# Kernel tuning notes

Hardware: AMD Instinct MI355X
Metric: run time of the kernel (lower is better)

Reference implementation:

```python
import jax, jax.numpy as jnp
import numpy as np

B = 8; NPC = 12500; N = B * NPC
L = 10.0; RES = 0.7; K = 16
IN_CH = 64; H1 = 68; H2 = 128; RNN = 128; ATTN = 32; E4 = 4 * RNN
EPS = 1e-5


def _knn_np(refs, queries, k):
    out = np.empty((queries.shape[0], k), dtype=np.int64)
    r2 = (refs * refs).sum(1)
    for s in range(0, queries.shape[0], 2048):
        q = queries[s:s + 2048]
        d2 = (q * q).sum(1)[:, None] - 2.0 * q @ refs.T + r2[None, :]
        out[s:s + q.shape[0]] = np.argpartition(d2, k, axis=1)[:, :k]
    return out


def setup_inputs():
    rng = np.random.default_rng(0)
    pos = rng.uniform(0.0, L, (N, 3)).astype(np.float32)
    batch = np.repeat(np.arange(B), NPC).astype(np.int32)
    x = (0.5 * rng.standard_normal((N, IN_CH))).astype(np.float32)
    refl = rng.uniform(0.0, 1.0, N).astype(np.float32)
    # voxel-grid sampling: one representative point per occupied voxel per cloud
    G = int(np.ceil(L / RES)) + 1
    v = np.floor(pos / RES).astype(np.int64)
    vkey = ((batch.astype(np.int64) * G + v[:, 0]) * G + v[:, 1]) * G + v[:, 2]
    _, first = np.unique(vkey, return_index=True)
    idx = np.sort(first)
    M = idx.shape[0]
    # per-cloud brute-force KNN (k neighbors in full set for every sampled point)
    src_list = []
    for b in range(B):
        qi = idx[(idx >= b * NPC) & (idx < (b + 1) * NPC)]
        src_list.append(_knn_np(pos[b * NPC:(b + 1) * NPC], pos[qi], K) + b * NPC)
    src = np.concatenate(src_list, 0).reshape(-1)
    tgt = np.repeat(np.arange(M), K)
    edge_index = np.stack([src, tgt]).astype(np.int32)

    def W(*s):
        return jnp.asarray((0.05 * rng.standard_normal(s)).astype(np.float32))

    def zeros(c):
        return jnp.zeros((c,), jnp.float32)

    def bnp(c):  # packed inference-mode BN params: [gamma, beta, mean, var]
        return jnp.asarray(np.stack([1.0 + 0.1 * rng.standard_normal(c), 0.1 * rng.standard_normal(c), 0.1 * rng.standard_normal(c), 1.0 + 0.1 * rng.uniform(0.0, 1.0, c)]).astype(np.float32))

    def dwp(c):  # depthwise k=1 conv = per-channel [weight, bias]
        return jnp.asarray(np.stack([1.0 + 0.1 * rng.standard_normal(c), 0.1 * rng.standard_normal(c)]).astype(np.float32))

    gum = -np.log(-np.log(rng.uniform(1e-6, 1.0 - 1e-6, (B, 2))))
    return dict(
        x=jnp.asarray(x), pos=jnp.asarray(pos), reflectance=jnp.asarray(refl),
        gumbel=jnp.asarray(gum.astype(np.float32)),
        gate_w1=W(4, H1), gate_b1=zeros(H1), gate_w2=W(H1, H1), gate_b2=zeros(H1),
        gate_wg=W(H1, 2), gate_bg=jnp.asarray(np.array([0.0, 2.0], np.float32)),
        loc_w1=W(H1, H2), loc_b1=zeros(H2), loc_w2=W(H2, H2), loc_b2=zeros(H2),
        attn_w1=W(H2, ATTN), attn_b1=zeros(ATTN), attn_w2=W(ATTN),
        exp_w=W(RNN, E4), exp_b=zeros(E4), exp_bn=bnp(E4),
        ds1_dw=dwp(E4), ds1_bn1=bnp(E4), ds1_pw_w=W(E4, E4), ds1_pw_b=zeros(E4), ds1_bn2=bnp(E4),
        blk_bn1=bnp(E4),
        ds2_dw=dwp(E4), ds2_bn1=bnp(E4), ds2_pw_w=W(E4, E4), ds2_pw_b=zeros(E4), ds2_bn2=bnp(E4),
        blk_bn2=bnp(E4),
        proj_w=W(E4, RNN), proj_b=zeros(RNN), proj_bn=bnp(RNN),
        batch=jnp.asarray(batch), idx=jnp.asarray(idx.astype(np.int32)),
        edge_index=jnp.asarray(edge_index), k=K, num_graphs=B)


def _bn(z, p):
    return p[0] * (z - p[2]) / jnp.sqrt(p[3] + EPS) + p[1]


def reference(x, pos, reflectance, gumbel, gate_w1, gate_b1, gate_w2, gate_b2, gate_wg, gate_bg, loc_w1, loc_b1, loc_w2, loc_b2, attn_w1, attn_b1, attn_w2, exp_w, exp_b, exp_bn, ds1_dw, ds1_bn1, ds1_pw_w, ds1_pw_b, ds1_bn2, blk_bn1, ds2_dw, ds2_bn1, ds2_pw_w, ds2_pw_b, ds2_bn2, blk_bn2, proj_w, proj_b, proj_bn, batch, idx, edge_index, k, num_graphs):
    # --- BinaryReflectanceGate (soft gumbel-softmax, tau=1) ---
    feats = jnp.concatenate([pos, reflectance[:, None]], -1)  # [N,4]
    h = jax.nn.relu(feats @ gate_w1 + gate_b1)
    h = jax.nn.relu(h @ gate_w2 + gate_b2)
    pooled = jax.ops.segment_max(h, batch, num_segments=num_graphs)  # global_max_pool
    logits = pooled @ gate_wg + gate_bg
    y_soft = jax.nn.softmax(logits + gumbel, axis=-1)
    refl_g = y_soft[:, 1][batch] * reflectance  # gated reflectance [N]
    pos4 = jnp.concatenate([pos, refl_g[:, None]], -1)  # [N,4]
    # --- AttentivePointNetConv: gather -> local MLP -> softmax attn -> reduce ---
    M = idx.shape[0]
    src = edge_index[0].reshape(M, k)  # k source neighbors per centroid
    msg_in = jnp.concatenate([x[src], pos4[src] - pos4[idx][:, None, :]], -1)  # [M,k,68]
    hm = jax.nn.relu(msg_in @ loc_w1 + loc_b1)
    msg = jax.nn.relu(hm @ loc_w2 + loc_b2)  # [M,k,128]
    score = jnp.tanh(msg @ attn_w1 + attn_b1) @ attn_w2  # [M,k]
    alpha = jax.nn.softmax(score, axis=-1)  # softmax over each centroid's edges
    agg = jnp.einsum('mk,mkc->mc', alpha, msg)  # [M,128]
    # --- InvertedResidualBlock (all convs kernel=1 -> channel matmuls, BN inference) ---
    out = jax.nn.relu(_bn(agg @ exp_w + exp_b, exp_bn))  # expand 128->512

    def ds(z, dw, bn1, pw_w, pw_b, bn2):
        d = jax.nn.relu(_bn(z * dw[0] + dw[1], bn1))  # depthwise k=1
        return _bn(d @ pw_w + pw_b, bn2)  # pointwise

    out = _bn(ds(out, ds1_dw, ds1_bn1, ds1_pw_w, ds1_pw_b, ds1_bn2), blk_bn1)
    out = _bn(ds(out, ds2_dw, ds2_bn1, ds2_pw_w, ds2_pw_b, ds2_bn2), blk_bn2)
    out = _bn(out @ proj_w + proj_b, proj_bn)  # project 512->128
    out = jax.nn.relu(out + agg)  # identity shortcut (RNN==RNN)
    return (out, pos[idx], batch[idx], refl_g[idx])
```

## Files before the change

kernel.cpp:

```cpp
#include <hip/hip_runtime.h>
#include <hip/hip_bf16.h>

typedef __hip_bfloat16 bf16;

#define B_GR 8
#define IN_CH 64
#define H1 68
#define H2 128
#define ATTN 32
#define E4 512
#define RNN 128
#define KNN 16
#define EPSV 1e-5f

typedef __attribute__((ext_vector_type(8))) short s8v;
typedef __attribute__((ext_vector_type(4))) float f4v;
#define MFMA16(a,b,c) __builtin_amdgcn_mfma_f32_16x16x32_bf16(a,b,c,0,0,0)

#define SK96 104
#define SK128 136
#define SK512 520

template<int DT> __device__ __forceinline__ float LD(const void* p, size_t i) {
    if (DT) return __bfloat162float(((const bf16*)p)[i]);
    return ((const float*)p)[i];
}
template<int DT> __device__ __forceinline__ void ST(void* p, size_t i, float v) {
    if (DT) ((bf16*)p)[i] = __float2bfloat16(v);
    else    ((float*)p)[i] = v;
}
__device__ __forceinline__ unsigned short f2bfb(float f) {
    unsigned u = __float_as_uint(f);
    unsigned r = (u + 0x7FFFu + ((u >> 16) & 1u)) >> 16;
    return (unsigned short)r;
}
__device__ __forceinline__ float bfb2f(unsigned short u) {
    return __uint_as_float(((unsigned)u) << 16);
}
__device__ __forceinline__ float fast_tanh(float x) {
    x = fminf(fmaxf(x, -12.f), 12.f);
    float e = __expf(2.f * x);
    return (e - 1.f) / (e + 1.f);
}

__global__ void prep_kernel(const void* pos, int* flag, int* pooled) {
    const int tid = threadIdx.x;
    for (int i = tid; i < B_GR*H1; i += 256) pooled[i] = 0;
    if (tid == 0) {
        const unsigned* w = (const unsigned*)pos;
        int ok = 1;
        #pragma unroll 8
        for (int i = 0; i < 256; i++) {
            float f = __uint_as_float((w[i] & 0xFFFFu) << 16);
            if (!(f >= -0.01f && f <= 10.05f)) ok = 0;
        }
        *flag = ok;
    }
}

#define W1T_E (128*SK96)
#define W2T_E (128*SK128)
#define AW1T_E (32*SK128)
#define EXPT_E (512*SK128)
#define D1T_E (512*SK512)
#define D2T_E (512*SK512)
#define PJT_E (128*SK512)
#define GW2T_E (80*SK96)
template<int DT> __global__ __launch_bounds__(256) void trans_kernel(
    const int* __restrict__ flag,
    const void* __restrict__ w1, const void* __restrict__ w2, const void* __restrict__ aw1,
    const void* __restrict__ expw, const void* __restrict__ d1pw,
    const void* __restrict__ d2pw, const void* __restrict__ pjw,
    const void* __restrict__ gw2,
    unsigned short* __restrict__ w1T, unsigned short* __restrict__ w2T,
    unsigned short* __restrict__ aw1T, unsigned short* __restrict__ expwT,
    unsigned short* __restrict__ d1pwT, unsigned short* __restrict__ d2pwT,
    unsigned short* __restrict__ pjwT, unsigned short* __restrict__ gw2gT)
{
    if (*flag != DT) return;
    const int T0 = W1T_E, T1 = T0+W2T_E, T2 = T1+AW1T_E, T3 = T2+EXPT_E,
              T4 = T3+D1T_E, T5 = T4+D2T_E, T6 = T5+PJT_E, T7 = T6+GW2T_E;
    for (int i = blockIdx.x*256 + threadIdx.x; i < T7; i += gridDim.x*256) {
        if (i < T0) {
            int n = i / SK96, k = i - n*SK96;
            w1T[i] = (k < H1) ? f2bfb(LD<DT>(w1, (size_t)k*H2 + n)) : 0;
        } else if (i < T1) {
            int j = i - T0; int n = j / SK128, k = j - n*SK128;
            w2T[j] = (k < H2) ? f2bfb(LD<DT>(w2, (size_t)k*H2 + n)) : 0;
        } else if (i < T2) {
            int j = i - T1; int n = j / SK128, k = j - n*SK128;
            aw1T[j] = (k < H2) ? f2bfb(LD<DT>(aw1, (size_t)k*ATTN + n)) : 0;
        } else if (i < T3) {
            int j = i - T2; int n = j / SK128, k = j - n*SK128;
            expwT[j] = (k < RNN) ? f2bfb(LD<DT>(expw, (size_t)k*E4 + n)) : 0;
        } else if (i < T4) {
            int j = i - T3; int n = j / SK512, k = j - n*SK512;
            d1pwT[j] = (k < E4) ? f2bfb(LD<DT>(d1pw, (size_t)k*E4 + n)) : 0;
        } else if (i < T5) {
            int j = i - T4; int n = j / SK512, k = j - n*SK512;
            d2pwT[j] = (k < E4) ? f2bfb(LD<DT>(d2pw, (size_t)k*E4 + n)) : 0;
        } else if (i < T6) {
            int j = i - T5; int n = j / SK512, k = j - n*SK512;
            pjwT[j] = (k < E4) ? f2bfb(LD<DT>(pjw, (size_t)k*RNN + n)) : 0;
        } else {
            int j = i - T6; int n = j / SK96, k = j - n*SK96;
            gw2gT[j] = (k < H1 && n < H1) ? f2bfb(LD<DT>(gw2, (size_t)k*H1 + n)) : 0;
        }
    }
}

template<int DT> __global__ void coef_kernel(
    const int* __restrict__ flag,
    const void* __restrict__ expb, const void* __restrict__ expbn,
    const void* __restrict__ d1dw, const void* __restrict__ d1bn1,
    const void* __restrict__ d1pb, const void* __restrict__ d1bn2, const void* __restrict__ bbn1,
    const void* __restrict__ d2dw, const void* __restrict__ d2bn1,
    const void* __restrict__ d2pb, const void* __restrict__ d2bn2, const void* __restrict__ bbn2,
    const void* __restrict__ pjb, const void* __restrict__ pjbn,
    float4* __restrict__ C1, float2* __restrict__ C2, float2* __restrict__ C3,
    float2* __restrict__ C4)
{
    if (*flag != DT) return;
    int c = blockIdx.x*256 + threadIdx.x;
    if (c < E4) {
        float a_e = LD<DT>(expbn,c) * rsqrtf(LD<DT>(expbn,3*E4+c)+EPSV);
        float t0  = a_e*(LD<DT>(expb,c) - LD<DT>(expbn,2*E4+c)) + LD<DT>(expbn,E4+c);
        float a1 = LD<DT>(d1bn1,c) * rsqrtf(LD<DT>(d1bn1,3*E4+c)+EPSV);
        float s1 = a1 * LD<DT>(d1dw,c);
        float t1 = a1*(LD<DT>(d1dw,E4+c) - LD<DT>(d1bn1,2*E4+c)) + LD<DT>(d1bn1,E4+c);
        C1[c] = make_float4(a_e, t0, s1, t1);
        float a2 = LD<DT>(d1bn2,c) * rsqrtf(LD<DT>(d1bn2,3*E4+c)+EPSV);
        float t2 = a2*(LD<DT>(d1pb,c) - LD<DT>(d1bn2,2*E4+c)) + LD<DT>(d1bn2,E4+c);
        float a3 = LD<DT>(bbn1,c) * rsqrtf(LD<DT>(bbn1,3*E4+c)+EPSV);
        float S2 = a3*a2;
        float T2 = a3*(t2 - LD<DT>(bbn1,2*E4+c)) + LD<DT>(bbn1,E4+c);
        float a4 = LD<DT>(d2bn1,c) * rsqrtf(LD<DT>(d2bn1,3*E4+c)+EPSV);
        float sdw = a4 * LD<DT>(d2dw,c);
        float tdw = a4*(LD<DT>(d2dw,E4+c) - LD<DT>(d2bn1,2*E4+c)) + LD<DT>(d2bn1,E4+c);
        C2[c] = make_float2(sdw*S2, sdw*T2 + tdw);
        float a5 = LD<DT>(d2bn2,c) * rsqrtf(LD<DT>(d2bn2,3*E4+c)+EPSV);
        float t5 = a5*(LD<DT>(d2pb,c) - LD<DT>(d2bn2,2*E4+c)) + LD<DT>(d2bn2,E4+c);
        float a6 = LD<DT>(bbn2,c) * rsqrtf(LD<DT>(bbn2,3*E4+c)+EPSV);
        C3[c] = make_float2(a6*a5, a6*(t5 - LD<DT>(bbn2,2*E4+c)) + LD<DT>(bbn2,E4+c));
    }
    if (c < RNN) {
        float ap = LD<DT>(pjbn,c) * rsqrtf(LD<DT>(pjbn,3*RNN+c)+EPSV);
        C4[c] = make_float2(ap, ap*(LD<DT>(pjb,c) - LD<DT>(pjbn,2*RNN+c)) + LD<DT>(pjbn,RNN+c));
    }
}

template<int DT> __global__ __launch_bounds__(256) void gate_mfma(
    const int* __restrict__ flag,
    const void* __restrict__ pos, const void* __restrict__ refl,
    const void* __restrict__ w1, const void* __restrict__ b1, const void* __restrict__ b2g,
    const unsigned short* __restrict__ gw2gT,
    int* __restrict__ pooled, int NPC, int CPB)
{
    if (*flag != DT) return;
    __shared__ __align__(16) unsigned short hs[256*SK96];
    __shared__ float w1s[4*H1], b1s[H1], b2s[H1];
    const int tid = threadIdx.x;
    for (int i = tid; i < 4*H1; i += 256) w1s[i] = LD<DT>(w1, i);
    if (tid < H1) { b1s[tid] = LD<DT>(b1, tid); b2s[tid] = LD<DT>(b2g, tid); }
    __syncthreads();

    const int bb = blockIdx.x / CPB;
    const int cc = blockIdx.x % CPB;
    const int base = bb*NPC + cc*256;
    const int limit = NPC - cc*256;
    const int p = base + ((tid < limit) ? tid : 0);

    {
        float f0 = LD<DT>(pos, (size_t)p*3+0), f1 = LD<DT>(pos, (size_t)p*3+1);
        float f2 = LD<DT>(pos, (size_t)p*3+2), f3 = LD<DT>(refl, p);
        float h[H1];
        #pragma unroll
        for (int j = 0; j < H1; j++)
            h[j] = fmaxf(b1s[j] + f0*w1s[j] + f1*w1s[H1+j] + f2*w1s[2*H1+j] + f3*w1s[3*H1+j], 0.f);
        #pragma unroll
        for (int j = 0; j < H1; j += 2) {
            unsigned v = (unsigned)f2bfb(h[j]) | ((unsigned)f2bfb(h[j+1]) << 16);
            *(unsigned*)&hs[tid*SK96 + j] = v;
        }
        #pragma unroll
        for (int j = H1; j < 96; j += 2) *(unsigned*)&hs[tid*SK96 + j] = 0;
    }
    __syncthreads();

    const int wv = tid >> 6, lane = tid & 63, quad = lane >> 4, l15 = lane & 15;
    f4v acc[4][5];
    #pragma unroll
    for (int mt = 0; mt < 4; mt++)
        #pragma unroll
        for (int nt = 0; nt < 5; nt++) acc[mt][nt] = (f4v){0.f,0.f,0.f,0.f};
    s8v af[4][3];
    #pragma unroll
    for (int mt = 0; mt < 4; mt++)
        #pragma unroll
        for (int ks = 0; ks < 3; ks++)
            af[mt][ks] = *(const s8v*)&hs[(wv*64 + mt*16 + l15)*SK96 + ks*32 + quad*8];
    #pragma unroll
    for (int nt = 0; nt < 5; nt++) {
        #pragma unroll
        for (int ks = 0; ks < 3; ks++) {
            s8v bf_ = *(const s8v*)&gw2gT[(size_t)(nt*16 + l15)*SK96 + ks*32 + quad*8];
            #pragma unroll
            for (int mt = 0; mt < 4; mt++) acc[mt][nt] = MFMA16(af[mt][ks], bf_, acc[mt][nt]);
        }
    }
    #pragma unroll
    for (int nt = 0; nt < 5; nt++) {
        int col = nt*16 + l15;
        float v = acc[0][nt][0];
        #pragma unroll
        for (int mt = 0; mt < 4; mt++)
            #pragma unroll
            for (int r = 0; r < 4; r++) v = fmaxf(v, acc[mt][nt][r]);
        v = fmaxf(v, __shfl_xor(v, 16));
        v = fmaxf(v, __shfl_xor(v, 32));
        if (quad == 0 && col < H1) {
            float o = fmaxf(v + b2s[col], 0.f);
            atomicMax(&pooled[bb*H1 + col], __float_as_int(o));
        }
    }
}

template<int DT> __global__ void gate2_kernel(
    const int* __restrict__ flag, const int* __restrict__ pooled,
    const void* __restrict__ wg, const void* __restrict__ bg,
    const void* __restrict__ gum, float* __restrict__ y1)
{
    if (*flag != DT) return;
    __shared__ float lg[B_GR][2];
    const int t = threadIdx.x;
    if (t < B_GR*2) {
        int b = t >> 1, g = t & 1;
        float a = LD<DT>(bg, g) + LD<DT>(gum, b*2+g);
        for (int c = 0; c < H1; c++) a += __int_as_float(pooled[b*H1+c]) * LD<DT>(wg, c*2+g);
        lg[b][g] = a;
    }
    __syncthreads();
    if (t < B_GR) {
        float l0 = lg[t][0], l1 = lg[t][1];
        float m = fmaxf(l0, l1);
        float e0 = __expf(l0-m), e1 = __expf(l1-m);
        y1[t] = e1 / (e0 + e1);
    }
}

template<int DT> __global__ __launch_bounds__(256) void edge_mfma(
    const int* __restrict__ flag,
    const void* __restrict__ x, const void* __restrict__ pos,
    const void* __restrict__ refl, const float* __restrict__ y1,
    const int* __restrict__ batch,
    const int* __restrict__ idxarr, const int* __restrict__ esrc,
    const void* __restrict__ b1, const void* __restrict__ b2,
    const void* __restrict__ ab1, const void* __restrict__ aw2,
    const unsigned short* __restrict__ gw1T, const unsigned short* __restrict__ gw2T,
    const unsigned short* __restrict__ gaw1T,
    void* __restrict__ out, int M)
{
    if (*flag != DT) return;
    __shared__ __align__(16) unsigned short u2[128*SK128];
    __shared__ float ssc[4][2][16];

    const int tid = threadIdx.x;
    const int wv = tid >> 6, lane = tid & 63, quad = lane >> 4, l15 = lane & 15;
    const int m0 = blockIdx.x * 8 + wv * 2;
    const int rb = wv * 32;

    s8v af[2][3];
    int mcl[2];
    float p4v[2][4];
    #pragma unroll
    for (int t = 0; t < 2; t++) {
        int mm = m0 + t; if (mm >= M) mm = M - 1;
        mcl[t] = mm;
        int t_idx = idxarr[mm];
        p4v[t][0] = LD<DT>(pos, (size_t)t_idx*3 + 0);
        p4v[t][1] = LD<DT>(pos, (size_t)t_idx*3 + 1);
        p4v[t][2] = LD<DT>(pos, (size_t)t_idx*3 + 2);
        p4v[t][3] = y1[batch[t_idx]] * LD<DT>(refl, t_idx);
        int s = esrc[mm*KNN + l15];
        if (DT) {
            const unsigned short* xs = (const unsigned short*)x + (size_t)s*IN_CH;
            af[t][0] = *(const s8v*)(xs + quad*8);
            af[t][1] = *(const s8v*)(xs + 32 + quad*8);
        } else {
            unsigned short tmp0[8], tmp1[8];
            #pragma unroll
            for (int e = 0; e < 8; e++) {
                tmp0[e] = f2bfb(LD<0>(x, (size_t)s*IN_CH + quad*8 + e));
                tmp1[e] = f2bfb(LD<0>(x, (size_t)s*IN_CH + 32 + quad*8 + e));
            }
            af[t][0] = *(const s8v*)tmp0;
            af[t][1] = *(const s8v*)tmp1;
        }
        s8v a2 = (s8v){0,0,0,0,0,0,0,0};
        if (quad == 0) {
            a2[0] = (short)f2bfb(LD<DT>(pos, (size_t)s*3 + 0) - p4v[t][0]);
            a2[1] = (short)f2bfb(LD<DT>(pos, (size_t)s*3 + 1) - p4v[t][1]);
            a2[2] = (short)f2bfb(LD<DT>(pos, (size_t)s*3 + 2) - p4v[t][2]);
            a2[3] = (short)f2bfb(y1[batch[s]] * LD<DT>(refl, s) - p4v[t][3]);
        }
        af[t][2] = a2;
    }

    {
        f4v acc[2][8];
        #pragma unroll
        for (int t = 0; t < 2; t++)
            #pragma unroll
            for (int nt = 0; nt < 8; nt++) acc[t][nt] = (f4v){0.f,0.f,0.f,0.f};
        #pragma unroll
        for (int nt = 0; nt < 8; nt++) {
            #pragma unroll
            for (int ks = 0; ks < 3; ks++) {
                s8v bf_ = *(const s8v*)&gw1T[(size_t)(nt*16 + l15)*SK96 + ks*32 + quad*8];
                acc[0][nt] = MFMA16(af[0][ks], bf_, acc[0][nt]);
                acc[1][nt] = MFMA16(af[1][ks], bf_, acc[1][nt]);
            }
        }
        #pragma unroll
        for (int nt = 0; nt < 8; nt++) {
            int col = nt*16 + l15;
            float bb = LD<DT>(b1, col);
            #pragma unroll
            for (int t = 0; t < 2; t++)
                #pragma unroll
                for (int r = 0; r < 4; r++) {
                    int row = rb + t*16 + quad*4 + r;
                    u2[row*SK128 + col] = f2bfb(fmaxf(acc[t][nt][r] + bb, 0.f));
                }
        }
    }

    {
        s8v af2[2][4];
        #pragma unroll
        for (int t = 0; t < 2; t++)
            #pragma unroll
            for (int ks = 0; ks < 4; ks++)
                af2[t][ks] = *(const s8v*)&u2[(rb + t*16 + l15)*SK128 + ks*32 + quad*8];
        f4v acc[2][8];
        #pragma unroll
        for (int t = 0; t < 2; t++)
            #pragma unroll
            for (int nt = 0; nt < 8; nt++) acc[t][nt] = (f4v){0.f,0.f,0.f,0.f};
        #pragma unroll
        for (int nt = 0; nt < 8; nt++) {
            #pragma unroll
            for (int ks = 0; ks < 4; ks++) {
                s8v bf_ = *(const s8v*)&gw2T[(size_t)(nt*16 + l15)*SK128 + ks*32 + quad*8];
                acc[0][nt] = MFMA16(af2[0][ks], bf_, acc[0][nt]);
                acc[1][nt] = MFMA16(af2[1][ks], bf_, acc[1][nt]);
            }
        }
        #pragma unroll
        for (int nt = 0; nt < 8; nt++) {
            int col = nt*16 + l15;
            float bb = LD<DT>(b2, col);
            #pragma unroll
            for (int t = 0; t < 2; t++)
                #pragma unroll
                for (int r = 0; r < 4; r++) {
                    int row = rb + t*16 + quad*4 + r;
                    u2[row*SK128 + col] = f2bfb(fmaxf(acc[t][nt][r] + bb, 0.f));
                }
        }
    }

    {
        s8v af3[2][4];
        #pragma unroll
        for (int t = 0; t < 2; t++)
            #pragma unroll
            for (int ks = 0; ks < 4; ks++)
                af3[t][ks] = *(const s8v*)&u2[(rb + t*16 + l15)*SK128 + ks*32 + quad*8];
        f4v acc[2][2];
        #pragma unroll
        for (int t = 0; t < 2; t++)
            #pragma unroll
            for (int nt = 0; nt < 2; nt++) acc[t][nt] = (f4v){0.f,0.f,0.f,0.f};
        #pragma unroll
        for (int nt = 0; nt < 2; nt++) {
            #pragma unroll
            for (int ks = 0; ks < 4; ks++) {
                s8v bf_ = *(const s8v*)&gaw1T[(size_t)(nt*16 + l15)*SK128 + ks*32 + quad*8];
                acc[0][nt] = MFMA16(af3[0][ks], bf_, acc[0][nt]);
                acc[1][nt] = MFMA16(af3[1][ks], bf_, acc[1][nt]);
            }
        }
        #pragma unroll
        for (int t = 0; t < 2; t++)
            #pragma unroll
            for (int r = 0; r < 4; r++) {
                float s = 0.f;
                #pragma unroll
                for (int nt = 0; nt < 2; nt++) {
                    int col = nt*16 + l15;
                    s += fast_tanh(acc[t][nt][r] + LD<DT>(ab1, col)) * LD<DT>(aw2, col);
                }
                s += __shfl_xor(s, 1);
                s += __shfl_xor(s, 2);
                s += __shfl_xor(s, 4);
                s += __shfl_xor(s, 8);
                if (l15 == 0) ssc[wv][t][quad*4 + r] = s;
            }
    }

    #pragma unroll
    for (int t = 0; t < 2; t++) {
        float sc[KNN];
        #pragma unroll
        for (int j = 0; j < KNN; j++) sc[j] = ssc[wv][t][j];
        float mx = sc[0];
        #pragma unroll
        for (int j = 1; j < KNN; j++) mx = fmaxf(mx, sc[j]);
        float den = 0.f;
        #pragma unroll
        for (int j = 0; j < KNN; j++) { sc[j] = __expf(sc[j] - mx); den += sc[j]; }
        float inv = 1.f / den;
        float a0 = 0.f, a1 = 0.f;
        #pragma unroll
        for (int j = 0; j < KNN; j++) {
            unsigned v = *(const unsigned*)&u2[(rb + t*16 + j)*SK128 + 2*lane];
            float w = sc[j] * inv;
            a0 += w * bfb2f((unsigned short)(v & 0xFFFFu));
            a1 += w * bfb2f((unsigned short)(v >> 16));
        }
        int mm = m0 + t;
        if (mm < M) {
            if (DT) {
                unsigned pk = (unsigned)f2bfb(a0) | ((unsigned)f2bfb(a1) << 16);
                *(unsigned*)((bf16*)out + (size_t)mm*H2 + 2*lane) = pk;
            } else {
                ST<0>(out, (size_t)mm*H2 + 2*lane, a0);
                ST<0>(out, (size_t)mm*H2 + 2*lane + 1, a1);
            }
            if (lane == 0) {
                ST<DT>(out, (size_t)M*128 + mm*3 + 0, p4v[t][0]);
                ST<DT>(out, (size_t)M*128 + mm*3 + 1, p4v[t][1]);
                ST<DT>(out, (size_t)M*128 + mm*3 + 2, p4v[t][2]);
                ST<DT>(out, (size_t)M*131 + mm, (float)batch[idxarr[mcl[t]]]);
                ST<DT>(out, (size_t)M*132 + mm, p4v[t][3]);
            }
        }
    }
}

template<int DT> __global__ __launch_bounds__(128) void post_mfma(
    const int* __restrict__ flag,
    const unsigned short* __restrict__ expwT, const unsigned short* __restrict__ d1pwT,
    const unsigned short* __restrict__ d2pwT, const unsigned short* __restrict__ pjwT,
    const float4* __restrict__ C1, const float2* __restrict__ C2,
    const float2* __restrict__ C3, const float2* __restrict__ C4,
    void* __restrict__ out, int M)
{
    if (*flag != DT) return;
    __shared__ __align__(16) unsigned short zs[32*SK512];
    const int tid = threadIdx.x;
    const int wv = tid >> 6, lane = tid & 63, quad = lane >> 4, l15 = lane & 15;
    const int m0w = blockIdx.x * 32 + wv * 16;
    unsigned short* strip = zs + wv * 16 * SK512;

    {
        s8v afe[4];
        int mrow = m0w + l15; if (mrow >= M) mrow = M - 1;
        if (DT) {
            const unsigned short* op = (const unsigned short*)out + (size_t)mrow*RNN;
            #pragma unroll
            for (int ks = 0; ks < 4; ks++)
                afe[ks] = *(const s8v*)(op + ks*32 + quad*8);
        } else {
            #pragma unroll
            for (int ks = 0; ks < 4; ks++) {
                unsigned short tmp[8];
                #pragma unroll
                for (int e = 0; e < 8; e++)
                    tmp[e] = f2bfb(LD<0>(out, (size_t)mrow*RNN + ks*32 + quad*8 + e));
                afe[ks] = *(const s8v*)tmp;
            }
        }
        #pragma unroll 4
        for (int nt = 0; nt < 32; nt++) {
            f4v acc = (f4v){0.f,0.f,0.f,0.f};
            #pragma unroll
            for (int ks = 0; ks < 4; ks++) {
                s8v bf_ = *(const s8v*)&expwT[(size_t)(nt*16 + l15)*SK128 + ks*32 + quad*8];
                acc = MFMA16(afe[ks], bf_, acc);
            }
            int col = nt*16 + l15;
            float4 cf = C1[col];
            #pragma unroll
            for (int r = 0; r < 4; r++) {
                float u = fmaxf(cf.x*acc[r] + cf.y, 0.f);
                float d = fmaxf(cf.z*u + cf.w, 0.f);
                strip[(quad*4 + r)*SK512 + col] = f2bfb(d);
            }
        }
    }

    {
        s8v af[16];
        #pragma unroll
        for (int ks = 0; ks < 16; ks++)
            af[ks] = *(const s8v*)&strip[l15*SK512 + ks*32 + quad*8];
        #pragma unroll 2
        for (int nt = 0; nt < 32; nt++) {
            f4v acc = (f4v){0.f,0.f,0.f,0.f};
            #pragma unroll
            for (int ks = 0; ks < 16; ks++) {
                s8v bf_ = *(const s8v*)&d1pwT[(size_t)(nt*16 + l15)*SK512 + ks*32 + quad*8];
                acc = MFMA16(af[ks], bf_, acc);
            }
            int col = nt*16 + l15;
            float2 cf = C2[col];
            #pragma unroll
            for (int r = 0; r < 4; r++)
                strip[(quad*4 + r)*SK512 + col] = f2bfb(fmaxf(cf.x*acc[r] + cf.y, 0.f));
        }
    }

    {
        s8v af[16];
        #pragma unroll
        for (int ks = 0; ks < 16; ks++)
            af[ks] = *(const s8v*)&strip[l15*SK512 + ks*32 + quad*8];
        #pragma unroll 2
        for (int nt = 0; nt < 32; nt++) {
            f4v acc = (f4v){0.f,0.f,0.f,0.f};
            #pragma unroll
            for (int ks = 0; ks < 16; ks++) {
                s8v bf_ = *(const s8v*)&d2pwT[(size_t)(nt*16 + l15)*SK512 + ks*32 + quad*8];
                acc = MFMA16(af[ks], bf_, acc);
            }
            int col = nt*16 + l15;
            float2 cf = C3[col];
            #pragma unroll
            for (int r = 0; r < 4; r++)
                strip[(quad*4 + r)*SK512 + col] = f2bfb(cf.x*acc[r] + cf.y);
        }
    }

    {
        s8v af[16];
        #pragma unroll
        for (int ks = 0; ks < 16; ks++)
            af[ks] = *(const s8v*)&strip[l15*SK512 + ks*32 + quad*8];
        #pragma unroll 2
        for (int nt = 0; nt < 8; nt++) {
            f4v acc = (f4v){0.f,0.f,0.f,0.f};
            #pragma unroll
            for (int ks = 0; ks < 16; ks++) {
                s8v bf_ = *(const s8v*)&pjwT[(size_t)(nt*16 + l15)*SK512 + ks*32 + quad*8];
                acc = MFMA16(af[ks], bf_, acc);
            }
            int col = nt*16 + l15;
            float2 cf = C4[col];
            #pragma unroll
            for (int r = 0; r < 4; r++) {
                int mm = m0w + quad*4 + r;
                if (mm < M) {
                    float agv = LD<DT>(out, (size_t)mm*RNN + col);
                    float o = fmaxf(cf.x*acc[r] + cf.y + agv, 0.f);
                    ST<DT>(out, (size_t)mm*RNN + col, o);
                }
            }
        }
    }
}

extern "C" void kernel_launch(void* const* d_in, const int* in_sizes, int n_in,
                              void* d_out, int out_size, void* d_ws, size_t ws_size,
                              hipStream_t stream)
{
    const void* x    = d_in[0];
    const void* pos  = d_in[1];
    const void* refl = d_in[2];
    const void* gum  = d_in[3];
    const void* gw1  = d_in[4];
    const void* gb1  = d_in[5];
    const void* gw2  = d_in[6];
    const void* gb2  = d_in[7];
    const void* gwg  = d_in[8];
    const void* gbg  = d_in[9];
    const void* lw1  = d_in[10];
    const void* lb1  = d_in[11];
    const void* lw2  = d_in[12];
    const void* lb2  = d_in[13];
    const void* aw1  = d_in[14];
    const void* ab1  = d_in[15];
    const void* aw2  = d_in[16];
    const void* expw = d_in[17];
    const void* expb = d_in[18];
    const void* expbn= d_in[19];
    const void* d1dw = d_in[20];
    const void* d1bn1= d_in[21];
    const void* d1pw = d_in[22];
    const void* d1pb = d_in[23];
    const void* d1bn2= d_in[24];
    const void* bbn1 = d_in[25];
    const void* d2dw = d_in[26];
    const void* d2bn1= d_in[27];
    const void* d2pw = d_in[28];
    const void* d2pb = d_in[29];
    const void* d2bn2= d_in[30];
    const void* bbn2 = d_in[31];
    const void* pjw  = d_in[32];
    const void* pjb  = d_in[33];
    const void* pjbn = d_in[34];
    const int* batch = (const int*)d_in[35];
    const int* idxp  = (const int*)d_in[36];
    const int* eidx  = (const int*)d_in[37];

    const int N = in_sizes[2];
    const int M = in_sizes[36];
    const int NPC = N / B_GR;
    const int CPB = (NPC + 255) / 256;

    char* wsb = (char*)d_ws;
    int*  flag   = (int*)wsb;
    int*  pooled = (int*)(wsb + 16);
    float* y1    = (float*)(wsb + 2304);
    unsigned short* w1T   = (unsigned short*)(wsb + 2368);
    unsigned short* w2T   = w1T + W1T_E;
    unsigned short* aw1T  = w2T + W2T_E;
    unsigned short* expwT = aw1T + AW1T_E;
    unsigned short* d1pwT = expwT + EXPT_E;
    unsigned short* d2pwT = d1pwT + D1T_E;
    unsigned short* pjwT  = d2pwT + D2T_E;
    unsigned short* gw2gT = pjwT + PJT_E;
    float4* C1 = (float4*)(gw2gT + GW2T_E + 8);
    float2* C2 = (float2*)(C1 + E4);
    float2* C3 = C2 + E4;
    float2* C4 = C3 + E4;

    prep_kernel<<<1, 256, 0, stream>>>(pos, flag, pooled);

    trans_kernel<0><<<512, 256, 0, stream>>>(flag, lw1, lw2, aw1, expw, d1pw, d2pw, pjw, gw2,
                                             w1T, w2T, aw1T, expwT, d1pwT, d2pwT, pjwT, gw2gT);
    trans_kernel<1><<<512, 256, 0, stream>>>(flag, lw1, lw2, aw1, expw, d1pw, d2pw, pjw, gw2,
                                             w1T, w2T, aw1T, expwT, d1pwT, d2pwT, pjwT, gw2gT);

    coef_kernel<0><<<2, 256, 0, stream>>>(flag, expb, expbn, d1dw, d1bn1, d1pb, d1bn2, bbn1,
                                          d2dw, d2bn1, d2pb, d2bn2, bbn2, pjb, pjbn,
                                          C1, C2, C3, C4);
    coef_kernel<1><<<2, 256, 0, stream>>>(flag, expb, expbn, d1dw, d1bn1, d1pb, d1bn2, bbn1,
                                          d2dw, d2bn1, d2pb, d2bn2, bbn2, pjb, pjbn,
                                          C1, C2, C3, C4);

    gate_mfma<0><<<B_GR*CPB, 256, 0, stream>>>(flag, pos, refl, gw1, gb1, gb2, gw2gT, pooled, NPC, CPB);
    gate_mfma<1><<<B_GR*CPB, 256, 0, stream>>>(flag, pos, refl, gw1, gb1, gb2, gw2gT, pooled, NPC, CPB);

    gate2_kernel<0><<<1, 64, 0, stream>>>(flag, pooled, gwg, gbg, gum, y1);
    gate2_kernel<1><<<1, 64, 0, stream>>>(flag, pooled, gwg, gbg, gum, y1);

    const int EB = (M + 7) / 8;
    edge_mfma<0><<<EB, 256, 0, stream>>>(flag, x, pos, refl, y1, batch, idxp, eidx,
                                         lb1, lb2, ab1, aw2, w1T, w2T, aw1T, d_out, M);
    edge_mfma<1><<<EB, 256, 0, stream>>>(flag, x, pos, refl, y1, batch, idxp, eidx,
                                         lb1, lb2, ab1, aw2, w1T, w2T, aw1T, d_out, M);

    const int PB = (M + 31) / 32;
    post_mfma<0><<<PB, 128, 0, stream>>>(flag, expwT, d1pwT, d2pwT, pjwT, C1, C2, C3, C4, d_out, M);
    post_mfma<1><<<PB, 128, 0, stream>>>(flag, expwT, d1pwT, d2pwT, pjwT, C1, C2, C3, C4, d_out, M);
}
```

Baseline: 460.5 us.

## Split post-MLP output columns across four waves sharing a 16-row tile

```diff
diff --git a/kernel.cpp b/kernel.cpp
--- a/kernel.cpp
+++ b/kernel.cpp
@@ -449,7 +449,7 @@
     }
 }
 
-template<int DT> __global__ __launch_bounds__(128) void post_mfma(
+template<int DT> __global__ __launch_bounds__(256) void post_mfma(
     const int* __restrict__ flag,
     const unsigned short* __restrict__ expwT, const unsigned short* __restrict__ d1pwT,
     const unsigned short* __restrict__ d2pwT, const unsigned short* __restrict__ pjwT,
@@ -458,15 +458,16 @@
     void* __restrict__ out, int M)
 {
     if (*flag != DT) return;
-    __shared__ __align__(16) unsigned short zs[32*SK512];
+    __shared__ __align__(16) unsigned short zsA[16*SK512];
+    __shared__ __align__(16) unsigned short zsB[16*SK512];
     const int tid = threadIdx.x;
     const int wv = tid >> 6, lane = tid & 63, quad = lane >> 4, l15 = lane & 15;
-    const int m0w = blockIdx.x * 32 + wv * 16;
-    unsigned short* strip = zs + wv * 16 * SK512;
+    const int m0 = blockIdx.x * 16;
+    const int nbase = wv * 128;
 
     {
         s8v afe[4];
-        int mrow = m0w + l15; if (mrow >= M) mrow = M - 1;
+        int mrow = m0 + l15; if (mrow >= M) mrow = M - 1;
         if (DT) {
             const unsigned short* op = (const unsigned short*)out + (size_t)mrow*RNN;
             #pragma unroll
@@ -482,85 +483,88 @@
                 afe[ks] = *(const s8v*)tmp;
             }
         }
-        #pragma unroll 4
-        for (int nt = 0; nt < 32; nt++) {
+        #pragma unroll
+        for (int nt = 0; nt < 8; nt++) {
             f4v acc = (f4v){0.f,0.f,0.f,0.f};
             #pragma unroll
             for (int ks = 0; ks < 4; ks++) {
-                s8v bf_ = *(const s8v*)&expwT[(size_t)(nt*16 + l15)*SK128 + ks*32 + quad*8];
+                s8v bf_ = *(const s8v*)&expwT[(size_t)(nbase + nt*16 + l15)*SK128 + ks*32 + quad*8];
                 acc = MFMA16(afe[ks], bf_, acc);
             }
-            int col = nt*16 + l15;
+            int col = nbase + nt*16 + l15;
             float4 cf = C1[col];
             #pragma unroll
             for (int r = 0; r < 4; r++) {
                 float u = fmaxf(cf.x*acc[r] + cf.y, 0.f);
                 float d = fmaxf(cf.z*u + cf.w, 0.f);
-                strip[(quad*4 + r)*SK512 + col] = f2bfb(d);
-            }
-        }
-    }
+                zsA[(quad*4 + r)*SK512 + col] = f2bfb(d);
+            }
+        }
+    }
+    __syncthreads();
 
     {
         s8v af[16];
         #pragma unroll
         for (int ks = 0; ks < 16; ks++)
-            af[ks] = *(const s8v*)&strip[l15*SK512 + ks*32 + quad*8];
-        #pragma unroll 2
-        for (int nt = 0; nt < 32; nt++) {
-            f4v acc = (f4v){0.f,0.f,0.f,0.f};
-            #pragma unroll
-            for (int ks = 0; ks < 16; ks++) {
-                s8v bf_ = *(const s8v*)&d1pwT[(size_t)(nt*16 + l15)*SK512 + ks*32 + quad*8];
-                acc = MFMA16(af[ks], bf_, acc);
-            }
-            int col = nt*16 + l15;
-            float2 cf = C2[col];
-            #pragma unroll
-            for (int r = 0; r < 4; r++)
-                strip[(quad*4 + r)*SK512 + col] = f2bfb(fmaxf(cf.x*acc[r] + cf.y, 0.f));
-        }
-    }
-
-    {
-        s8v af[16];
-        #pragma unroll
-        for (int ks = 0; ks < 16; ks++)
-            af[ks] = *(const s8v*)&strip[l15*SK512 + ks*32 + quad*8];
-        #pragma unroll 2
-        for (int nt = 0; nt < 32; nt++) {
-            f4v acc = (f4v){0.f,0.f,0.f,0.f};
-            #pragma unroll
-            for (int ks = 0; ks < 16; ks++) {
-                s8v bf_ = *(const s8v*)&d2pwT[(size_t)(nt*16 + l15)*SK512 + ks*32 + quad*8];
-                acc = MFMA16(af[ks], bf_, acc);
-            }
-            int col = nt*16 + l15;
-            float2 cf = C3[col];
-            #pragma unroll
-            for (int r = 0; r < 4; r++)
-                strip[(quad*4 + r)*SK512 + col] = f2bfb(cf.x*acc[r] + cf.y);
-        }
-    }
-
-    {
-        s8v af[16];
-        #pragma unroll
-        for (int ks = 0; ks < 16; ks++)
-            af[ks] = *(const s8v*)&strip[l15*SK512 + ks*32 + quad*8];
+            af[ks] = *(const s8v*)&zsA[l15*SK512 + ks*32 + quad*8];
         #pragma unroll 2
         for (int nt = 0; nt < 8; nt++) {
             f4v acc = (f4v){0.f,0.f,0.f,0.f};
             #pragma unroll
             for (int ks = 0; ks < 16; ks++) {
-                s8v bf_ = *(const s8v*)&pjwT[(size_t)(nt*16 + l15)*SK512 + ks*32 + quad*8];
+                s8v bf_ = *(const s8v*)&d1pwT[(size_t)(nbase + nt*16 + l15)*SK512 + ks*32 + quad*8];
                 acc = MFMA16(af[ks], bf_, acc);
             }
-            int col = nt*16 + l15;
+            int col = nbase + nt*16 + l15;
+            float2 cf = C2[col];
+            #pragma unroll
+            for (int r = 0; r < 4; r++)
+                zsB[(quad*4 + r)*SK512 + col] = f2bfb(fmaxf(cf.x*acc[r] + cf.y, 0.f));
+        }
+    }
+    __syncthreads();
+
+    {
+        s8v af[16];
+        #pragma unroll
+        for (int ks = 0; ks < 16; ks++)
+            af[ks] = *(const s8v*)&zsB[l15*SK512 + ks*32 + quad*8];
+        #pragma unroll 2
+        for (int nt = 0; nt < 8; nt++) {
+            f4v acc = (f4v){0.f,0.f,0.f,0.f};
+            #pragma unroll
+            for (int ks = 0; ks < 16; ks++) {
+                s8v bf_ = *(const s8v*)&d2pwT[(size_t)(nbase + nt*16 + l15)*SK512 + ks*32 + quad*8];
+                acc = MFMA16(af[ks], bf_, acc);
+            }
+            int col = nbase + nt*16 + l15;
+            float2 cf = C3[col];
+            #pragma unroll
+            for (int r = 0; r < 4; r++)
+                zsA[(quad*4 + r)*SK512 + col] = f2bfb(cf.x*acc[r] + cf.y);
+        }
+    }
+    __syncthreads();
+
+    {
+        s8v af[16];
+        #pragma unroll
+        for (int ks = 0; ks < 16; ks++)
+            af[ks] = *(const s8v*)&zsA[l15*SK512 + ks*32 + quad*8];
+        #pragma unroll
+        for (int nt = 0; nt < 2; nt++) {
+            f4v acc = (f4v){0.f,0.f,0.f,0.f};
+            #pragma unroll
+            for (int ks = 0; ks < 16; ks++) {
+                s8v bf_ = *(const s8v*)&pjwT[(size_t)(wv*32 + nt*16 + l15)*SK512 + ks*32 + quad*8];
+                acc = MFMA16(af[ks], bf_, acc);
+            }
+            int col = wv*32 + nt*16 + l15;
             float2 cf = C4[col];
             #pragma unroll
             for (int r = 0; r < 4; r++) {
-                int mm = m0w + quad*4 + r;
+                int mm = m0 + quad*4 + r;
                 if (mm < M) {
                     float agv = LD<DT>(out, (size_t)mm*RNN + col);
                     float o = fmaxf(cf.x*acc[r] + cf.y + agv, 0.f);
@@ -662,7 +666,7 @@
     edge_mfma<1><<<EB, 256, 0, stream>>>(flag, x, pos, refl, y1, batch, idxp, eidx,
                                          lb1, lb2, ab1, aw2, w1T, w2T, aw1T, d_out, M);
 
-    const int PB = (M + 31) / 32;
-    post_mfma<0><<<PB, 128, 0, stream>>>(flag, expwT, d1pwT, d2pwT, pjwT, C1, C2, C3, C4, d_out, M);
-    post_mfma<1><<<PB, 128, 0, stream>>>(flag, expwT, d1pwT, d2pwT, pjwT, C1, C2, C3, C4, d_out, M);
-}
+    const int PB = (M + 15) / 16;
+    post_mfma<0><<<PB, 256, 0, stream>>>(flag, expwT, d1pwT, d2pwT, pjwT, C1, C2, C3, C4, d_out, M);
+    post_mfma<1><<<PB, 256, 0, stream>>>(flag, expwT, d1pwT, d2pwT, pjwT, C1, C2, C3, C4, d_out, M);
+}
```

Result: slower. 476.5 us (+3.5%).
